# Optimization experiments

Hardware: AMD Instinct MI355X
Metric: run time of the kernel (lower is better)

Reference implementation:

```python
import jax, jax.numpy as jnp
import numpy as np

N, C, T, V = 32, 64, 512, 25
CO = 64            # out_channels
C4 = CO // 4       # inter channel (conv_a/conv_d output, kc//3)
W3 = 3 * V         # unfolded node dim
BN_EPS = 1e-5


def setup_inputs() -> dict:
    key = jax.random.key(0)
    ks = jax.random.split(key, 12)
    s = 0.05
    return {
        "x": jax.random.normal(ks[0], (N, C, T, V), dtype=jnp.float32),
        "A": jax.random.uniform(ks[1], (3, W3, W3), dtype=jnp.float32) * 0.1,  # fixed adjacency buffer
        "PA": jnp.full((3, W3, W3), 1e-6, dtype=jnp.float32),                   # learned adjacency offset
        "conv_a_w": jax.random.normal(ks[2], (C4, C), dtype=jnp.float32) * s,   # 1x1 conv_a[0]
        "conv_a_b": jnp.zeros((C4,), dtype=jnp.float32),
        "conv_d_w": jax.random.normal(ks[3], (C4, C), dtype=jnp.float32) * s,   # 1x1 conv_d[0]
        "conv_d_b": jnp.zeros((C4,), dtype=jnp.float32),
        "conv_w": jax.random.normal(ks[4], (3 * C4, C), dtype=jnp.float32) * s, # main 1x1 conv (t_kernel_size=1)
        "conv_b": jnp.zeros((3 * C4,), dtype=jnp.float32),
        "out_w": jax.random.normal(ks[5], (CO, C4, 3), dtype=jnp.float32) * s,  # conv3d kernel (1,3,1)
        "out_b": jnp.zeros((CO,), dtype=jnp.float32),
        "bn_gamma": jnp.ones((CO,), dtype=jnp.float32),
        "bn_beta": jnp.zeros((CO,), dtype=jnp.float32),
        "bn_mean": jnp.zeros((CO,), dtype=jnp.float32),
        "bn_var": jnp.ones((CO,), dtype=jnp.float32),
    }


def _unfold3(x):
    # UnfoldTemporalWindows(3,1,1): (N,C,T,V) -> (N,C,T,3V), zero-pad T by 1
    n, c, t, v = x.shape
    xp = jnp.pad(x, ((0, 0), (0, 0), (1, 1), (0, 0)))
    win = jnp.stack([xp[:, :, i:i + t, :] for i in range(3)], axis=3)  # (N,C,T,3,V)
    return win.reshape(n, c, t, 3 * v)


def reference(x, A, PA, conv_a_w, conv_a_b, conv_d_w, conv_d_b,
              conv_w, conv_b, out_w, out_b, bn_gamma, bn_beta, bn_mean, bn_var):
    n, c, t, v = x.shape
    w3 = 3 * v
    Aeff = A + PA  # (3, 3V, 3V)

    x2 = _unfold3(x)  # (N,C,T,3V)

    # adaptive graph attention: matmul-softmax-matmul
    a1 = jnp.einsum('nctw,oc->notw', x2, conv_a_w) + conv_a_b[None, :, None, None]  # (N,C4,T,3V)
    a11 = a1.transpose(0, 3, 1, 2).reshape(n, w3, -1)   # (N,3V,C4*T)
    a2 = a1.reshape(n, -1, w3)                          # (N,C4*T,3V)
    att = jax.nn.softmax(jnp.matmul(a11, a2) / w3, axis=-2)  # (N,3V,3V), softmax over dim -2
    xz = jnp.matmul(x2.reshape(n, c * t, w3), att).reshape(n, c, t, w3)
    z = jnp.einsum('nctw,oc->notw', xz, conv_d_w) + conv_d_b[None, :, None, None]  # (N,C4,T,3V)

    # main branch: 1x1 conv -> split into k=3 -> einsum graph conv with A
    x1 = jnp.einsum('nctw,oc->notw', x2, conv_w) + conv_b[None, :, None, None]  # (N,3*C4,T,3V)
    c4 = conv_d_w.shape[0]
    x1 = x1.reshape(n, 3, c4, t, w3)
    x1 = jnp.einsum('nkctv,kvw->nctw', x1, Aeff)  # (N,C4,T,3V)
    x1 = x1 + z

    # conv3d (1,3,1) collapses the window-of-3 dim
    x1 = x1.reshape(n, c4, t, 3, v)
    y = jnp.einsum('nctwv,ocw->notv', x1, out_w) + out_b[None, :, None, None]  # (N,CO,T,V)

    # BatchNorm2d (inference form)
    inv = jax.lax.rsqrt(bn_var + BN_EPS)
    y = (y - bn_mean[None, :, None, None]) * (bn_gamma * inv)[None, :, None, None] + bn_beta[None, :, None, None]

    y = y + x  # in_channels == out_channels -> identity residual
    return jax.nn.relu(y)
```

## Files before the change

kernel.cpp:

```cpp
#include <hip/hip_runtime.h>
#include <hip/hip_bf16.h>


typedef unsigned short u16;
typedef unsigned int   u32;
typedef __attribute__((ext_vector_type(8))) short bf16x8;
typedef __attribute__((ext_vector_type(4))) float f32x4;

__device__ __forceinline__ float b2f(u32 u) {
    union { u32 i; float f; } x; x.i = (u & 0xffffu) << 16; return x.f;
}
__device__ __forceinline__ u16 f2b(float f) {
    union { float f; u32 i; } x; x.f = f;
    u32 i = x.i;
    return (u16)((i + 0x7fffu + ((i >> 16) & 1u)) >> 16);
}
__device__ __forceinline__ u32 pack2(float a, float b) {
    return (u32)f2b(a) | ((u32)f2b(b) << 16);
}

__global__ __launch_bounds__(256) void k0_bta(
    const float* __restrict__ A, const float* __restrict__ PA,
    u16* __restrict__ BtA)
{
    int e = blockIdx.x * 256 + threadIdx.x;
    if (e >= 80 * 288) return;
    int w = e / 288, k = e - w * 288;
    int r = k >> 5, v = k & 31, g = r / 3, i = r - g * 3;
    float val = 0.f;
    if (v < 25 && w < 75) {
        int idx = (g * 75 + i * 25 + v) * 75 + w;
        val = A[idx] + PA[idx];
    }
    BtA[e] = f2b(val);
}

__global__ __launch_bounds__(256, 2) void k1_conv80(
    const float* __restrict__ x,
    const float* __restrict__ wa, const float* __restrict__ ba,
    const float* __restrict__ wd, const float* __restrict__ bd,
    const float* __restrict__ wc, const float* __restrict__ bc,
    u16* __restrict__ a1o, u16* __restrict__ hcn)
{
    __shared__ __align__(16) u16 Xt[256 * 64];
    __shared__ __align__(16) u16 Csh[80 * 264];
    char* XtB = (char*)Xt;

    const int b    = blockIdx.x;
    const int n    = b >> 4;
    const int t0   = (b & 15) << 5;
    const int tid  = threadIdx.x;
    const int wave = tid >> 6, lane = tid & 63;
    const int q    = lane >> 4, r = lane & 15;

    bf16x8 wfrag[5][2];
    float  breg[5];
    #pragma unroll
    for (int mt = 0; mt < 5; ++mt) {
        const int o = mt * 16 + r;
        const float* src = (o < 16) ? (wa + o * 64)
                         : (o < 32) ? (wd + (o - 16) * 64)
                                    : (wc + (o - 32) * 64);
        breg[mt] = (o < 16) ? ba[o] : (o < 32) ? bd[o - 16] : bc[o - 32];
        #pragma unroll
        for (int ks = 0; ks < 2; ++ks) {
            bf16x8 f;
            #pragma unroll
            for (int j = 0; j < 8; ++j)
                f[j] = (short)f2b(src[ks * 32 + q * 8 + j]);
            wfrag[mt][ks] = f;
        }
    }

    if (t0 == 0) {
        uint4 z; z.x = 0u; z.y = 0u; z.z = 0u; z.w = 0u;
        for (int e = tid; e < 50; e += 256)
            *(uint4*)&a1o[((size_t)n * 514) * 400 + e * 8] = z;
    }
    if (t0 == 480) {
        uint4 z; z.x = 0u; z.y = 0u; z.z = 0u; z.w = 0u;
        for (int e = tid; e < 50; e += 256)
            *(uint4*)&a1o[((size_t)n * 514 + 513) * 400 + e * 8] = z;
    }

    {
        uint4 z; z.x = 0u; z.y = 0u; z.z = 0u; z.w = 0u;
        for (int e = tid; e < 448; e += 256) {
            const int pc = e >> 3, ch = e & 7;
            const int tl = pc / 7, pv = pc - tl * 7;
            const int col = tl * 32 + 25 + pv;
            *(uint4*)(XtB + col * 128 + ch * 16) = z;
        }
    }

    auto epilogue = [&](int tbp) {
        for (int e = tid; e < 2048; e += 256) {
            const int cc  = e >> 5;
            const int rem = e & 31;
            const int tl  = rem >> 2, v0 = (rem & 3) << 3;
            const int o   = (cc < 48) ? cc + 32 : cc - 32;
            uint4 pk = *(const uint4*)&Csh[o * 264 + tl * 32 + v0];
            *(uint4*)&hcn[(((size_t)n * 64 + cc) * 512 + (tbp + tl)) * 32 + v0] = pk;
        }
        for (int e = tid; e < 400; e += 256) {
            const int tv = e >> 1, h = (e & 1) << 3;
            const int tl = (tv * 41) >> 10;
            const int v  = tv - tl * 25;
            const int cb = tl * 32 + v;
            u16 a[8];
            #pragma unroll
            for (int k = 0; k < 8; ++k) a[k] = Csh[(h + k) * 264 + cb];
            uint4 pk;
            pk.x = (u32)a[0] | ((u32)a[1] << 16);
            pk.y = (u32)a[2] | ((u32)a[3] << 16);
            pk.z = (u32)a[4] | ((u32)a[5] << 16);
            pk.w = (u32)a[6] | ((u32)a[7] << 16);
            *(uint4*)&a1o[(((size_t)n * 514 + (tbp + tl + 1)) * 25 + v) * 16 + h] = pk;
        }
    };

    for (int s = 0; s < 4; ++s) {
        const int tb = t0 + s * 8;

        if (s > 0) epilogue(tb - 8);
        for (int e = tid; e < 400; e += 256) {
            const int co = e / 50;
            const int tq = e - co * 50;
            const float* gp = x + (((size_t)n * 64 + co * 8) * 512 + tb) * 25 + tq * 4;
            float fl[32];
            #pragma unroll
            for (int i = 0; i < 8; ++i) {
                const float4 t4 = *(const float4*)(gp + (size_t)i * 12800);
                fl[i * 4 + 0] = t4.x; fl[i * 4 + 1] = t4.y;
                fl[i * 4 + 2] = t4.z; fl[i * 4 + 3] = t4.w;
            }
            #pragma unroll
            for (int j = 0; j < 4; ++j) {
                const int tv  = tq * 4 + j;
                const int tl  = (tv * 41) >> 10;
                const int col = tl * 32 + (tv - tl * 25);
                uint4 pk;
                pk.x = pack2(fl[0 * 4 + j], fl[1 * 4 + j]);
                pk.y = pack2(fl[2 * 4 + j], fl[3 * 4 + j]);
                pk.z = pack2(fl[4 * 4 + j], fl[5 * 4 + j]);
                pk.w = pack2(fl[6 * 4 + j], fl[7 * 4 + j]);
                *(uint4*)(XtB + col * 128 + ((co * 16) ^ ((col & 7) << 4))) = pk;
            }
        }
        __syncthreads();

        {
            f32x4 acc[4][5];
            #pragma unroll
            for (int a_ = 0; a_ < 4; ++a_)
                #pragma unroll
                for (int m_ = 0; m_ < 5; ++m_)
                    acc[a_][m_] = (f32x4){0.f, 0.f, 0.f, 0.f};

            #pragma unroll
            for (int nt4 = 0; nt4 < 4; ++nt4) {
                const int col = (wave * 4 + nt4) * 16 + r;
                const int swz = (col & 7) << 4;
                const char* rowp = (const char*)Xt + col * 128;
                const bf16x8 x0 = *(const bf16x8*)(rowp + ((q * 16) ^ swz));
                const bf16x8 x1 = *(const bf16x8*)(rowp + ((64 + q * 16) ^ swz));
                #pragma unroll
                for (int mt = 0; mt < 5; ++mt) {
                    acc[nt4][mt] = __builtin_amdgcn_mfma_f32_16x16x32_bf16(
                        x0, wfrag[mt][0], acc[nt4][mt], 0, 0, 0);
                    acc[nt4][mt] = __builtin_amdgcn_mfma_f32_16x16x32_bf16(
                        x1, wfrag[mt][1], acc[nt4][mt], 0, 0, 0);
                }
            }
            #pragma unroll
            for (int nt4 = 0; nt4 < 4; ++nt4) {
                const int colb = (wave * 4 + nt4) * 16 + q * 4;
                #pragma unroll
                for (int mt = 0; mt < 5; ++mt) {
                    const int o = mt * 16 + r;
                    const float bi = breg[mt];
                    uint2 pr;
                    pr.x = pack2(acc[nt4][mt][0] + bi, acc[nt4][mt][1] + bi);
                    pr.y = pack2(acc[nt4][mt][2] + bi, acc[nt4][mt][3] + bi);
                    *(uint2*)&Csh[o * 264 + colb] = pr;
                }
            }
        }
        __syncthreads();
    }
    epilogue(t0 + 24);
}

__global__ __launch_bounds__(256, 2) void k2a_mfma(
    const u16* __restrict__ a1o, float* __restrict__ Spart)
{
    __shared__ u16 U[80 * 136];
    __shared__ float Sred[80 * 80];
    __shared__ float Sred2[80 * 80];
    const int b   = blockIdx.x;
    const int n   = b >> 4;
    const int tc  = b & 15;
    const int t0  = tc * 32;
    const int tid = threadIdx.x;
    const int wave = tid >> 6, lane = tid & 63;
    const int q = lane >> 4, col = lane & 15;

    f32x4 acc[25];
    #pragma unroll
    for (int i = 0; i < 25; ++i) acc[i] = (f32x4){0.f, 0.f, 0.f, 0.f};

    for (int s = 0; s < 4; ++s) {
        __syncthreads();
        for (int e = tid; e < 1280; e += 256) {
            int row = e >> 4, c8 = (e & 15) << 3;
            uint4 val; val.x = 0u; val.y = 0u; val.z = 0u; val.w = 0u;
            if (row < 75) {
                int i = row / 25, v = row - i * 25;
                int tl = c8 >> 4, o0 = c8 & 8;
                int tp = t0 + s * 8 + tl + i;
                val = *(const uint4*)&a1o[(((size_t)n * 514 + tp) * 25 + v) * 16 + o0];
            }
            *(uint4*)&U[row * 136 + c8] = val;
        }
        __syncthreads();

        const int k0 = wave * 32 + q * 8;
        bf16x8 fr[5];
        #pragma unroll
        for (int r = 0; r < 5; ++r)
            fr[r] = *(const bf16x8*)&U[(r * 16 + col) * 136 + k0];
        #pragma unroll
        for (int mt = 0; mt < 5; ++mt)
            #pragma unroll
            for (int nt = 0; nt < 5; ++nt)
                acc[mt * 5 + nt] = __builtin_amdgcn_mfma_f32_16x16x32_bf16(
                    fr[mt], fr[nt], acc[mt * 5 + nt], 0, 0, 0);
    }

    if (wave < 2) {
        float* S = (wave == 0) ? Sred : Sred2;
        #pragma unroll
        for (int mt = 0; mt < 5; ++mt)
            #pragma unroll
            for (int nt = 0; nt < 5; ++nt)
                #pragma unroll
                for (int reg = 0; reg < 4; ++reg)
                    S[(mt * 16 + q * 4 + reg) * 80 + nt * 16 + col] =
                        acc[mt * 5 + nt][reg];
    }
    __syncthreads();
    if (wave >= 2) {
        float* S = (wave == 2) ? Sred : Sred2;
        #pragma unroll
        for (int mt = 0; mt < 5; ++mt)
            #pragma unroll
            for (int nt = 0; nt < 5; ++nt)
                #pragma unroll
                for (int reg = 0; reg < 4; ++reg)
                    S[(mt * 16 + q * 4 + reg) * 80 + nt * 16 + col] +=
                        acc[mt * 5 + nt][reg];
    }
    __syncthreads();
    float* dst = &Spart[(size_t)(n * 16 + tc) * 6400];
    for (int e = tid; e < 6400; e += 256) dst[e] = Sred[e] + Sred2[e];
}

__global__ __launch_bounds__(256) void k2b_softmax(
    const float* __restrict__ Spart, u16* __restrict__ BtT)
{
    __shared__ float S2[75][17];
    const int b = blockIdx.x;
    const int n = b / 5, w2g = b - n * 5;
    const int w2base = w2g * 16;
    const int tid = threadIdx.x;

    for (int e = tid; e < 1200; e += 256) {
        const int w1 = e >> 4, w2l = e & 15;
        const float* sp = &Spart[(size_t)(n * 16) * 6400 + w1 * 80 + w2base + w2l];
        float s = 0.f;
        #pragma unroll
        for (int ks = 0; ks < 16; ++ks) s += sp[(size_t)ks * 6400];
        S2[w1][w2l] = s * (1.0f / 75.0f);
    }
    __syncthreads();

    const int w2l = tid >> 4, j = tid & 15;
    float m = -1e30f;
    for (int w1 = j; w1 < 75; w1 += 16) m = fmaxf(m, S2[w1][w2l]);
    #pragma unroll
    for (int off = 8; off; off >>= 1) m = fmaxf(m, __shfl_xor(m, off, 16));
    float s = 0.f;
    for (int w1 = j; w1 < 75; w1 += 16) {
        const float e = __expf(S2[w1][w2l] - m);
        S2[w1][w2l] = e;
        s += e;
    }
    #pragma unroll
    for (int off = 8; off; off >>= 1) s += __shfl_xor(s, off, 16);
    const float r = 1.0f / s;
    for (int w1 = j; w1 < 75; w1 += 16) S2[w1][w2l] *= r;
    __syncthreads();

    for (int e = tid; e < 1536; e += 256) {
        const int wl = e / 96, k = e - wl * 96;
        const int i = k >> 5, v = k & 31;
        const int w2 = w2base + wl;
        const float val = (w2 < 75 && v < 25) ? S2[i * 25 + v][wl] : 0.f;
        BtT[((size_t)n * 80 + w2) * 96 + k] = f2b(val);
    }
}

__global__ __launch_bounds__(256, 2) void k3_graph(
    const u16* __restrict__ hcn, const u16* __restrict__ BtA,
    const u16* __restrict__ BtT, u16* __restrict__ sum12)
{
    __shared__ u16 Bt[80 * 392];
    const int b    = blockIdx.x;
    const int n    = b >> 4;
    const int tblk = (b & 15) << 5;
    const int tid  = threadIdx.x;

    for (int e = tid; e < 3840; e += 256) {
        int row = e / 48, cs = e - row * 48;
        uint4 val;
        if (cs < 36) val = *(const uint4*)&BtA[row * 288 + cs * 8];
        else         val = *(const uint4*)&BtT[((size_t)n * 80 + row) * 96 + (cs - 36) * 8];
        *(uint4*)&Bt[row * 392 + cs * 8] = val;
    }
    __syncthreads();

    const int wave = tid >> 6, lane = tid & 63;
    const int c = lane & 15, q = lane >> 4;
    const int tb = tblk + wave * 8;

    auto hload = [&](int g, int tp) -> bf16x8 {
        if (tp < 0 || tp >= 512) return (bf16x8)(short)0;
        const size_t rowb = ((size_t)n * 64 + g * 16 + c) * 512;
        return *(const bf16x8*)&hcn[(rowb + tp) * 32 + q * 8];
    };

    bf16x8 frag[4][4];
    #pragma unroll
    for (int g = 0; g < 4; ++g) {
        frag[g][0] = hload(g, tb - 1);
        frag[g][1] = hload(g, tb);
        frag[g][2] = hload(g, tb + 1);
        frag[g][3] = hload(g, tb + 2);
    }

    #pragma unroll
    for (int tt = 0; tt < 8; tt += 2) {
        const int t0 = tb + tt, t1 = t0 + 1;
        #pragma unroll 1
        for (int nt = 0; nt < 5; ++nt) {
            f32x4 acc0 = {0.f, 0.f, 0.f, 0.f};
            f32x4 acc1 = {0.f, 0.f, 0.f, 0.f};
            const u16* bp = &Bt[(nt * 16 + c) * 392 + q * 8];
            #pragma unroll
            for (int g = 0; g < 4; ++g)
                #pragma unroll
                for (int i = 0; i < 3; ++i) {
                    const int r = g * 3 + i;
                    bf16x8 bf = *(const bf16x8*)(bp + r * 32);
                    acc0 = __builtin_amdgcn_mfma_f32_16x16x32_bf16(bf, frag[g][i],     acc0, 0, 0, 0);
                    acc1 = __builtin_amdgcn_mfma_f32_16x16x32_bf16(bf, frag[g][i + 1], acc1, 0, 0, 0);
                }
            const size_t tb0 = ((size_t)n * 512 + t0) * 1200;
            const size_t tb1 = ((size_t)n * 512 + t1) * 1200;
            #pragma unroll
            for (int reg = 0; reg < 4; ++reg) {
                const int w = nt * 16 + q * 4 + reg;
                if (w < 75) {
                    const int ww = (w >= 50) ? 2 : ((w >= 25) ? 1 : 0);
                    const int v  = w - ww * 25;
                    const int off = (v * 3 + ww) * 16 + c;
                    sum12[tb0 + off] = f2b(acc0[reg]);
                    sum12[tb1 + off] = f2b(acc1[reg]);
                }
            }
        }
        if (tt < 6) {
            #pragma unroll
            for (int g = 0; g < 4; ++g) {
                frag[g][0] = frag[g][2];
                frag[g][1] = frag[g][3];
                frag[g][2] = hload(g, t0 + 3);
                frag[g][3] = hload(g, t0 + 4);
            }
        }
    }
}

__global__ __launch_bounds__(256, 3) void k4_out(
    const u16* __restrict__ sum12,
    const float* __restrict__ ow, const float* __restrict__ obias,
    const float* __restrict__ bg, const float* __restrict__ bb,
    const float* __restrict__ bm, const float* __restrict__ bv,
    const float* __restrict__ x, float* __restrict__ out)
{
    __shared__ __align__(16) char smem[64 * 204 * 4];
    u16*   Bsh = (u16*)smem;
    float* Csh = (float*)smem;
    char*  BshB = smem;

    const int b    = blockIdx.x;
    const int n    = b >> 6;
    const int t0   = (b & 63) << 3;
    const int tid  = threadIdx.x;
    const int wave = tid >> 6, lane = tid & 63;
    const int q    = lane >> 4, c15 = lane & 15;

    {
        uint4 z; z.x = 0u; z.y = 0u; z.z = 0u; z.w = 0u;
        for (int e = tid; e < 960; e += 256) {
            int col, j;
            if (e < 512) { col = e >> 1; j = 6 + (e & 1); }
            else {
                const int r2 = e - 512;
                const int cc = r2 >> 3; j = r2 & 7;
                const int tl = cc / 7, pv = cc - tl * 7;
                col = tl * 32 + 25 + pv;
            }
            *(uint4*)(BshB + col * 128 + ((j * 16) ^ ((col & 7) << 4))) = z;
        }
    }
    for (int e = tid; e < 1200; e += 256) {
        const int j  = e % 6;
        const int rv = e / 6;
        const int tl = (rv * 41) >> 10;
        const int v  = rv - tl * 25;
        const uint4 val = *(const uint4*)
            &sum12[((size_t)n * 512 + t0 + tl) * 1200 + v * 48 + j * 8];
        const int col = tl * 32 + v;
        *(uint4*)(BshB + col * 128 + ((j * 16) ^ ((col & 7) << 4))) = val;
    }

    bf16x8 wfrag[4][2];
    #pragma unroll
    for (int mt = 0; mt < 4; ++mt) {
        const int o = mt * 16 + c15;
        #pragma unroll
        for (int ks = 0; ks < 2; ++ks) {
            bf16x8 f;
            #pragma unroll
            for (int j = 0; j < 8; ++j) {
                const int k = ks * 32 + q * 8 + j;
                const int cc = k & 15, ww = k >> 4;
                f[j] = (k < 48) ? (short)f2b(ow[o * 48 + cc * 3 + ww]) : (short)0;
            }
            wfrag[mt][ks] = f;
        }
    }
    float scl[4][4], shf2[4][4];
    #pragma unroll
    for (int mt = 0; mt < 4; ++mt)
        #pragma unroll
        for (int reg = 0; reg < 4; ++reg) {
            const int o = mt * 16 + q * 4 + reg;
            const float s = bg[o] * rsqrtf(bv[o] + 1e-5f);
            scl[mt][reg]  = s;
            shf2[mt][reg] = bb[o] + (obias[o] - bm[o]) * s;
        }
    __syncthreads();

    f32x4 acc[4][4];
    #pragma unroll
    for (int ct = 0; ct < 4; ++ct)
        #pragma unroll
        for (int mt = 0; mt < 4; ++mt)
            acc[ct][mt] = (f32x4){0.f, 0.f, 0.f, 0.f};

    const int wb = wave * 64;
    #pragma unroll
    for (int ct = 0; ct < 4; ++ct) {
        const int col = wb + ct * 16 + c15;
        const int swz = (col & 7) << 4;
        const char* rp = BshB + col * 128;
        const bf16x8 b0 = *(const bf16x8*)(rp + ((q * 16) ^ swz));
        const bf16x8 b1 = *(const bf16x8*)(rp + ((64 + q * 16) ^ swz));
        #pragma unroll
        for (int mt = 0; mt < 4; ++mt) {
            acc[ct][mt] = __builtin_amdgcn_mfma_f32_16x16x32_bf16(
                wfrag[mt][0], b0, acc[ct][mt], 0, 0, 0);
            acc[ct][mt] = __builtin_amdgcn_mfma_f32_16x16x32_bf16(
                wfrag[mt][1], b1, acc[ct][mt], 0, 0, 0);
        }
    }
    __syncthreads();

    #pragma unroll
    for (int ct = 0; ct < 4; ++ct) {
        const int col = wb + ct * 16 + c15;
        const int tl = col >> 5, v = col & 31;
        if (v < 25) {
            const int cc = tl * 25 + v;
            #pragma unroll
            for (int mt = 0; mt < 4; ++mt)
                #pragma unroll
                for (int reg = 0; reg < 4; ++reg) {
                    const int o = mt * 16 + q * 4 + reg;
                    Csh[o * 204 + cc] =
                        acc[ct][mt][reg] * scl[mt][reg] + shf2[mt][reg];
                }
        }
    }
    __syncthreads();

    for (int e = tid; e < 3200; e += 256) {
        const int o = e / 50, jj = e - o * 50;
        const size_t gidx = (((size_t)n * 64 + o) * 512 + t0) * 25 + jj * 4;
        const float4 xv = *(const float4*)&x[gidx];
        const float* cp = &Csh[o * 204 + jj * 4];
        float4 yv;
        yv.x = fmaxf(cp[0] + xv.x, 0.f);
        yv.y = fmaxf(cp[1] + xv.y, 0.f);
        yv.z = fmaxf(cp[2] + xv.z, 0.f);
        yv.w = fmaxf(cp[3] + xv.w, 0.f);
        *(float4*)&out[gidx] = yv;
    }
}

extern "C" void kernel_launch(void* const* d_in, const int* in_sizes, int n_in,
                              void* d_out, int out_size, void* d_ws, size_t ws_size,
                              hipStream_t stream)
{
    const float* x  = (const float*)d_in[0];
    const float* A  = (const float*)d_in[1];
    const float* PA = (const float*)d_in[2];
    const float* wa = (const float*)d_in[3];
    const float* ba = (const float*)d_in[4];
    const float* wd = (const float*)d_in[5];
    const float* bd = (const float*)d_in[6];
    const float* wc = (const float*)d_in[7];
    const float* bc = (const float*)d_in[8];
    const float* ow = (const float*)d_in[9];
    const float* ob = (const float*)d_in[10];
    const float* bg = (const float*)d_in[11];
    const float* bb = (const float*)d_in[12];
    const float* bm = (const float*)d_in[13];
    const float* bv = (const float*)d_in[14];
    float* out = (float*)d_out;

    char* ws = (char*)d_ws;
    u16*   a1o   = (u16*)(ws);
    u16*   hcn   = (u16*)(ws + 13158400);
    u16*   sum12 = (u16*)(ws + 80267264);
    float* Spart = (float*)(ws + 80267264);
    u16*   BtA   = (u16*)(ws + 130598912);
    u16*   BtT   = (u16*)(ws + 130644992);

    k0_bta    <<<90,   256, 0, stream>>>(A, PA, BtA);
    k1_conv80 <<<512,  256, 0, stream>>>(x, wa, ba, wd, bd, wc, bc, a1o, hcn);
    k2a_mfma  <<<512,  256, 0, stream>>>(a1o, Spart);
    k2b_softmax<<<160, 256, 0, stream>>>(Spart, BtT);
    k3_graph  <<<512,  256, 0, stream>>>(hcn, BtA, BtT, sum12);
    k4_out    <<<2048, 256, 0, stream>>>(sum12, ow, ob, bg, bb, bm, bv, x, out);
}
```

Baseline: 389.5 us.

## Fuse graph-conv and output-conv kernels through an LDS tile

The graph-convolution kernel and the output conv/BN/residual kernel are merged into one kernel. Each block now computes the graph-conv result for 8 timesteps into a shared-memory tile and consumes it directly, so the bf16 sum12 intermediate is no longer written to and read back from global memory. In exchange, the grid has four times as many blocks, and each block reloads the 62 KB Bt matrix from L2. Each wave also loads four hcn timesteps to produce two outputs, which adds redundant input reads. The larger LDS footprint may also limit occupancy.

```diff
diff --git a/kernel.cpp b/kernel.cpp
--- a/kernel.cpp
+++ b/kernel.cpp
@@ -310,15 +310,25 @@
     }
 }
 
-__global__ __launch_bounds__(256, 2) void k3_graph(
+__global__ __launch_bounds__(256, 2) void k34_fused(
     const u16* __restrict__ hcn, const u16* __restrict__ BtA,
-    const u16* __restrict__ BtT, u16* __restrict__ sum12)
+    const u16* __restrict__ BtT,
+    const float* __restrict__ ow, const float* __restrict__ obias,
+    const float* __restrict__ bg, const float* __restrict__ bb,
+    const float* __restrict__ bm, const float* __restrict__ bv,
+    const float* __restrict__ x, float* __restrict__ out)
 {
-    __shared__ u16 Bt[80 * 392];
+    __shared__ __align__(16) char smem[81920];
+    u16*   Bt   = (u16*)smem;
+    u16*   tile = (u16*)(smem + 62720);
+    float* Csh  = (float*)smem;
+
     const int b    = blockIdx.x;
-    const int n    = b >> 4;
-    const int tblk = (b & 15) << 5;
+    const int n    = b >> 6;
+    const int t0   = (b & 63) << 3;
     const int tid  = threadIdx.x;
+    const int wave = tid >> 6, lane = tid & 63;
+    const int q    = lane >> 4, c15 = lane & 15;
 
     for (int e = tid; e < 3840; e += 256) {
         int row = e / 48, cs = e - row * 48;
@@ -329,110 +339,43 @@
     }
     __syncthreads();
 
-    const int wave = tid >> 6, lane = tid & 63;
-    const int c = lane & 15, q = lane >> 4;
-    const int tb = tblk + wave * 8;
-
-    auto hload = [&](int g, int tp) -> bf16x8 {
-        if (tp < 0 || tp >= 512) return (bf16x8)(short)0;
-        const size_t rowb = ((size_t)n * 64 + g * 16 + c) * 512;
-        return *(const bf16x8*)&hcn[(rowb + tp) * 32 + q * 8];
-    };
-
-    bf16x8 frag[4][4];
-    #pragma unroll
-    for (int g = 0; g < 4; ++g) {
-        frag[g][0] = hload(g, tb - 1);
-        frag[g][1] = hload(g, tb);
-        frag[g][2] = hload(g, tb + 1);
-        frag[g][3] = hload(g, tb + 2);
-    }
-
-    #pragma unroll
-    for (int tt = 0; tt < 8; tt += 2) {
-        const int t0 = tb + tt, t1 = t0 + 1;
+    {
+        const int tp = t0 + 2 * wave;
+        bf16x8 frag[4][4];
+        #pragma unroll
+        for (int g = 0; g < 4; ++g)
+            #pragma unroll
+            for (int s2 = 0; s2 < 4; ++s2) {
+                const int t = tp - 1 + s2;
+                frag[g][s2] = (t >= 0 && t < 512)
+                    ? *(const bf16x8*)&hcn[(((size_t)n * 64 + g * 16 + c15) * 512 + t) * 32 + q * 8]
+                    : (bf16x8)(short)0;
+            }
         #pragma unroll 1
         for (int nt = 0; nt < 5; ++nt) {
             f32x4 acc0 = {0.f, 0.f, 0.f, 0.f};
             f32x4 acc1 = {0.f, 0.f, 0.f, 0.f};
-            const u16* bp = &Bt[(nt * 16 + c) * 392 + q * 8];
+            const u16* bp = &Bt[(nt * 16 + c15) * 392 + q * 8];
             #pragma unroll
             for (int g = 0; g < 4; ++g)
                 #pragma unroll
                 for (int i = 0; i < 3; ++i) {
-                    const int r = g * 3 + i;
-                    bf16x8 bf = *(const bf16x8*)(bp + r * 32);
+                    bf16x8 bf = *(const bf16x8*)(bp + (g * 3 + i) * 32);
                     acc0 = __builtin_amdgcn_mfma_f32_16x16x32_bf16(bf, frag[g][i],     acc0, 0, 0, 0);
                     acc1 = __builtin_amdgcn_mfma_f32_16x16x32_bf16(bf, frag[g][i + 1], acc1, 0, 0, 0);
                 }
-            const size_t tb0 = ((size_t)n * 512 + t0) * 1200;
-            const size_t tb1 = ((size_t)n * 512 + t1) * 1200;
             #pragma unroll
             for (int reg = 0; reg < 4; ++reg) {
                 const int w = nt * 16 + q * 4 + reg;
                 if (w < 75) {
                     const int ww = (w >= 50) ? 2 : ((w >= 25) ? 1 : 0);
                     const int v  = w - ww * 25;
-                    const int off = (v * 3 + ww) * 16 + c;
-                    sum12[tb0 + off] = f2b(acc0[reg]);
-                    sum12[tb1 + off] = f2b(acc1[reg]);
+                    const int off = (v * 3 + ww) * 16 + c15;
+                    tile[(2 * wave)     * 1200 + off] = f2b(acc0[reg]);
+                    tile[(2 * wave + 1) * 1200 + off] = f2b(acc1[reg]);
                 }
             }
         }
-        if (tt < 6) {
-            #pragma unroll
-            for (int g = 0; g < 4; ++g) {
-                frag[g][0] = frag[g][2];
-                frag[g][1] = frag[g][3];
-                frag[g][2] = hload(g, t0 + 3);
-                frag[g][3] = hload(g, t0 + 4);
-            }
-        }
-    }
-}
-
-__global__ __launch_bounds__(256, 3) void k4_out(
-    const u16* __restrict__ sum12,
-    const float* __restrict__ ow, const float* __restrict__ obias,
-    const float* __restrict__ bg, const float* __restrict__ bb,
-    const float* __restrict__ bm, const float* __restrict__ bv,
-    const float* __restrict__ x, float* __restrict__ out)
-{
-    __shared__ __align__(16) char smem[64 * 204 * 4];
-    u16*   Bsh = (u16*)smem;
-    float* Csh = (float*)smem;
-    char*  BshB = smem;
-
-    const int b    = blockIdx.x;
-    const int n    = b >> 6;
-    const int t0   = (b & 63) << 3;
-    const int tid  = threadIdx.x;
-    const int wave = tid >> 6, lane = tid & 63;
-    const int q    = lane >> 4, c15 = lane & 15;
-
-    {
-        uint4 z; z.x = 0u; z.y = 0u; z.z = 0u; z.w = 0u;
-        for (int e = tid; e < 960; e += 256) {
-            int col, j;
-            if (e < 512) { col = e >> 1; j = 6 + (e & 1); }
-            else {
-                const int r2 = e - 512;
-                const int cc = r2 >> 3; j = r2 & 7;
-                const int tl = cc / 7, pv = cc - tl * 7;
-                col = tl * 32 + 25 + pv;
-            }
-            *(uint4*)(BshB + col * 128 + ((j * 16) ^ ((col & 7) << 4))) = z;
-        }
-    }
-    for (int e = tid; e < 1200; e += 256) {
-        const int j  = e % 6;
-        const int rv = e / 6;
-        const int tl = (rv * 41) >> 10;
-        const int v  = rv - tl * 25;
-        const uint4 val = *(const uint4*)
-            &sum12[((size_t)n * 512 + t0 + tl) * 1200 + v * 48 + j * 8];
-        const int col = tl * 32 + v;
-        *(uint4*)(BshB + col * 128 + ((j * 16) ^ ((col & 7) << 4))) = val;
     }
 
     bf16x8 wfrag[4][2];
@@ -471,13 +414,15 @@
             acc[ct][mt] = (f32x4){0.f, 0.f, 0.f, 0.f};
 
     const int wb = wave * 64;
+    const int ww0 = q >> 1, cs2 = (q & 1) * 8;
     #pragma unroll
     for (int ct = 0; ct < 4; ++ct) {
         const int col = wb + ct * 16 + c15;
-        const int swz = (col & 7) << 4;
-        const char* rp = BshB + col * 128;
-        const bf16x8 b0 = *(const bf16x8*)(rp + ((q * 16) ^ swz));
-        const bf16x8 b1 = *(const bf16x8*)(rp + ((64 + q * 16) ^ swz));
+        const int tl = col >> 5, v = col & 31;
+        const int vv = (v < 25) ? v : 0;
+        const u16* trow = tile + tl * 1200;
+        const bf16x8 b0 = *(const bf16x8*)&trow[(vv * 3 + ww0) * 16 + cs2];
+        const bf16x8 b1 = *(const bf16x8*)&trow[(vv * 3 + 2) * 16 + cs2];
         #pragma unroll
         for (int mt = 0; mt < 4; ++mt) {
             acc[ct][mt] = __builtin_amdgcn_mfma_f32_16x16x32_bf16(
@@ -486,7 +431,6 @@
                 wfrag[mt][1], b1, acc[ct][mt], 0, 0, 0);
         }
     }
-    __syncthreads();
 
     #pragma unroll
     for (int ct = 0; ct < 4; ++ct) {
@@ -544,7 +488,6 @@
     char* ws = (char*)d_ws;
     u16*   a1o   = (u16*)(ws);
     u16*   hcn   = (u16*)(ws + 13158400);
-    u16*   sum12 = (u16*)(ws + 80267264);
     float* Spart = (float*)(ws + 80267264);
     u16*   BtA   = (u16*)(ws + 130598912);
     u16*   BtT   = (u16*)(ws + 130644992);
@@ -553,6 +496,5 @@
     k1_conv80 <<<512,  256, 0, stream>>>(x, wa, ba, wd, bd, wc, bc, a1o, hcn);
     k2a_mfma  <<<512,  256, 0, stream>>>(a1o, Spart);
     k2b_softmax<<<160, 256, 0, stream>>>(Spart, BtT);
-    k3_graph  <<<512,  256, 0, stream>>>(hcn, BtA, BtT, sum12);
-    k4_out    <<<2048, 256, 0, stream>>>(sum12, ow, ob, bg, bb, bm, bv, x, out);
-}
+    k34_fused <<<2048, 256, 0, stream>>>(hcn, BtA, BtT, ow, ob, bg, bb, bm, bv, x, out);
+}
```

New measurement: 380.7 us. 2.3% less time.
